# Kernel optimization log

Hardware: AMD Instinct MI355X
Metric: run time of the kernel (lower is better)

Reference implementation:

```python
import jax, jax.numpy as jnp
import numpy as np

D_MODEL, D_K, C_DIM = 1024, 64, 64
B, S = 4, 4096


def setup_inputs() -> dict:
    key = jax.random.key(0)
    ks = jax.random.split(key, 10)
    sc = 1.0 / np.sqrt(D_MODEL)
    return {
        "X": jax.random.normal(ks[0], (B, S, D_MODEL), jnp.float32),
        "cultural_embedding": jax.random.normal(ks[1], (B, C_DIM), jnp.float32),
        "WQ": jax.random.normal(ks[2], (D_MODEL, D_K), jnp.float32) * sc,
        "bQ": jnp.zeros((D_K,), jnp.float32),
        "WK": jax.random.normal(ks[3], (D_MODEL, D_K), jnp.float32) * sc,
        "bK": jnp.zeros((D_K,), jnp.float32),
        "WV": jax.random.normal(ks[4], (D_MODEL, D_K), jnp.float32) * sc,
        "bV": jnp.zeros((D_K,), jnp.float32),
        "WC": jax.random.normal(ks[5], (C_DIM, D_K), jnp.float32) * (1.0 / np.sqrt(C_DIM)),
        "bC": jnp.zeros((D_K,), jnp.float32),
        "lam": jnp.float32(1.0),
    }


def reference(X, cultural_embedding, WQ, bQ, WK, bK, WV, bV, WC, bC, lam):
    # Projections: [B,S,d_k]
    Q = jnp.einsum('bsm,mk->bsk', X, WQ) + bQ
    K = jnp.einsum('bsm,mk->bsk', X, WK) + bK
    V = jnp.einsum('bsm,mk->bsk', X, WV) + bV
    # Cultural projection: [B,d_k]
    c_proj = cultural_embedding @ WC + bC
    # Base attention logits [B,S,S]
    base_logits = jnp.einsum('bqk,bsk->bqs', Q, K) / jnp.sqrt(jnp.float32(D_K))
    # Rank-1 cultural bias per query row, scalar lambda gate
    cultural_bias = lam * jnp.einsum('bsd,bd->bs', Q, c_proj)  # [B,S]
    combined = base_logits + cultural_bias[..., None]
    attn = jax.nn.softmax(combined, axis=-1)
    return jnp.einsum('bqs,bsk->bqk', attn, V)
```

## Files before the change

kernel.cpp:

```cpp
#include <hip/hip_runtime.h>

#define B_  4
#define S_  4096
#define DM  1024
#define DK  64
#define NSPLIT 8
#define KSPAN (S_ / NSPLIT)
#define QT  256

typedef _Float16 half8  __attribute__((ext_vector_type(8)));
typedef _Float16 half4v __attribute__((ext_vector_type(4)));
typedef float    floatx4 __attribute__((ext_vector_type(4)));

#define QSCALE 0.18033688011112042f
#define EXP2F(x) __builtin_amdgcn_exp2f(x)

__global__ __launch_bounds__(256) void wt_kernel(
    const float* __restrict__ WQ, const float* __restrict__ WK,
    const float* __restrict__ WV, _Float16* __restrict__ Wt2)
{
    const int proj = blockIdx.y;
    const float* W = (proj == 0) ? WQ : (proj == 1) ? WK : WV;
    const int k0 = blockIdx.x * 64;
    const int t = threadIdx.x;
    __shared__ float T[64][68];

    #pragma unroll
    for (int p = 0; p < 4; p++) {
        int c = p * 256 + t;
        int k = c >> 4, n4 = (c & 15) * 4;
        float4 v = *(const float4*)(W + (size_t)(k0 + k) * DK + n4);
        T[k][n4 + 0] = v.x; T[k][n4 + 1] = v.y;
        T[k][n4 + 2] = v.z; T[k][n4 + 3] = v.w;
    }
    __syncthreads();

    const int n = t >> 2, kc = (t & 3) * 16;
    half8 h0, h1;
    #pragma unroll
    for (int j = 0; j < 8; j++) h0[j] = (_Float16)T[kc + j][n];
    #pragma unroll
    for (int j = 0; j < 8; j++) h1[j] = (_Float16)T[kc + 8 + j][n];
    _Float16* dst = Wt2 + (((size_t)blockIdx.x * 3 + proj) * 64 + n) * 64 + kc;
    *(half8*)(dst)     = h0;
    *(half8*)(dst + 8) = h1;
}

__global__ __launch_bounds__(256) void proj_mfma_kernel(
    const float* __restrict__ X, const _Float16* __restrict__ Wt2,
    const float* __restrict__ bQ, const float* __restrict__ bK,
    const float* __restrict__ bV,
    _Float16* __restrict__ Qh, _Float16* __restrict__ Kh,
    _Float16* __restrict__ Vt)
{
    const int t    = threadIdx.x;
    const int wave = t >> 6, lane = t & 63;
    const int quad = lane >> 4, l15 = lane & 15;
    const int row0 = blockIdx.x * 64 + wave * 16;

    const float* xp = X + (size_t)(row0 + l15) * DM + quad * 8;

    floatx4 acc[3][4];
    #pragma unroll
    for (int pr = 0; pr < 3; pr++)
        #pragma unroll
        for (int nt = 0; nt < 4; nt++)
            acc[pr][nt] = (floatx4){0.f, 0.f, 0.f, 0.f};

    float4 xa = *(const float4*)(xp + 0);
    float4 xb = *(const float4*)(xp + 4);
    float4 xc = *(const float4*)(xp + 32);
    float4 xd = *(const float4*)(xp + 36);

    for (int kt = 0; kt < DM / 64; kt++) {
        half8 xf0, xf1;
        xf0[0] = (_Float16)xa.x; xf0[1] = (_Float16)xa.y;
        xf0[2] = (_Float16)xa.z; xf0[3] = (_Float16)xa.w;
        xf0[4] = (_Float16)xb.x; xf0[5] = (_Float16)xb.y;
        xf0[6] = (_Float16)xb.z; xf0[7] = (_Float16)xb.w;
        xf1[0] = (_Float16)xc.x; xf1[1] = (_Float16)xc.y;
        xf1[2] = (_Float16)xc.z; xf1[3] = (_Float16)xc.w;
        xf1[4] = (_Float16)xd.x; xf1[5] = (_Float16)xd.y;
        xf1[6] = (_Float16)xd.z; xf1[7] = (_Float16)xd.w;

        if (kt + 1 < DM / 64) {
            const int kn = (kt + 1) * 64;
            xa = *(const float4*)(xp + kn + 0);
            xb = *(const float4*)(xp + kn + 4);
            xc = *(const float4*)(xp + kn + 32);
            xd = *(const float4*)(xp + kn + 36);
        }

        const _Float16* wb =
            Wt2 + ((size_t)kt * 3 * 64) * 64 + (size_t)l15 * 64 + quad * 8;
        #pragma unroll
        for (int pr = 0; pr < 3; pr++) {
            #pragma unroll
            for (int nt = 0; nt < 4; nt++) {
                const _Float16* wp = wb + (size_t)(pr * 64 + nt * 16) * 64;
                half8 w0 = *(const half8*)(wp);
                half8 w1 = *(const half8*)(wp + 32);
                floatx4 a = acc[pr][nt];
                a = __builtin_amdgcn_mfma_f32_16x16x32_f16(xf0, w0, a, 0, 0, 0);
                a = __builtin_amdgcn_mfma_f32_16x16x32_f16(xf1, w1, a, 0, 0, 0);
                acc[pr][nt] = a;
            }
        }
    }

    float bqv[4], bkv[4], bvv[4];
    #pragma unroll
    for (int nt = 0; nt < 4; nt++) {
        bqv[nt] = bQ[nt * 16 + l15];
        bkv[nt] = bK[nt * 16 + l15];
        bvv[nt] = bV[nt * 16 + l15];
    }

    const int orow = row0 + quad * 4;
    const int bidx = row0 >> 12;
    const int s0   = (row0 & (S_ - 1)) + quad * 4;
    #pragma unroll
    for (int nt = 0; nt < 4; nt++) {
        const int d = nt * 16 + l15;
        #pragma unroll
        for (int i = 0; i < 4; i++) {
            Qh[(size_t)(orow + i) * DK + d] =
                (_Float16)((acc[0][nt][i] + bqv[nt]) * QSCALE);
            Kh[(size_t)(orow + i) * DK + d] =
                (_Float16)(acc[1][nt][i] + bkv[nt]);
        }
        half4v hv;
        #pragma unroll
        for (int i = 0; i < 4; i++)
            hv[i] = (_Float16)(acc[2][nt][i] + bvv[nt]);
        *(half4v*)(Vt + (size_t)bidx * DK * S_ + (size_t)d * S_ + s0) = hv;
    }
}

__global__ __launch_bounds__(512, 4) void flash_mfma_kernel(
    const _Float16* __restrict__ Qh, const _Float16* __restrict__ Kh,
    const _Float16* __restrict__ Vt, _Float16* __restrict__ Oph,
    float* __restrict__ Lp)
{
    const int b     = blockIdx.y;
    const int q0    = blockIdx.x * QT;
    const int split = blockIdx.z;
    const int kbase = split * KSPAN;
    const int t     = threadIdx.x;
    const int wave  = t >> 6, lane = t & 63;
    const int quad  = lane >> 4, l15 = lane & 15;

    __shared__ __align__(16) _Float16 Ks[64 * 72];
    __shared__ __align__(16) _Float16 Vs[64 * 72];
    __shared__ __align__(16) _Float16 QsPs[QT * 72];

    const _Float16* Qb = Qh + ((size_t)b * S_ + q0) * DK;
    const _Float16* Kb = Kh + ((size_t)b * S_ + kbase) * DK;
    const _Float16* Vb = Vt + (size_t)b * DK * S_ + kbase;

    #pragma unroll
    for (int p = 0; p < 4; p++) {
        int c = p * 512 + t;
        int r = c >> 3, col = (c & 7) * 8;
        *(half8*)&QsPs[r * 72 + col] = *(const half8*)(Qb + r * 64 + col);
    }
    __syncthreads();
    half8 qf0[2], qf1[2];
    #pragma unroll
    for (int mt = 0; mt < 2; mt++) {
        const int r = wave * 32 + mt * 16 + l15;
        qf0[mt] = *(half8*)&QsPs[r * 72 + quad * 8];
        qf1[mt] = *(half8*)&QsPs[r * 72 + 32 + quad * 8];
    }
    __syncthreads();

    _Float16* Pw = &QsPs[wave * 32 * 72];

    floatx4 acc[2][4];
    float rs[2][4];
    #pragma unroll
    for (int mt = 0; mt < 2; mt++) {
        #pragma unroll
        for (int nt = 0; nt < 4; nt++) acc[mt][nt] = (floatx4){0.f,0.f,0.f,0.f};
        #pragma unroll
        for (int i = 0; i < 4; i++) rs[mt][i] = 0.f;
    }

    const int kr = t >> 3, kcol = (t & 7) * 8;
    half8 kreg = *(const half8*)(Kb + (size_t)kr * DK + kcol);
    half8 vreg = *(const half8*)(Vb + (size_t)kr * S_ + kcol);

    for (int k0 = 0; k0 < KSPAN; k0 += 64) {
        __syncthreads();
        *(half8*)&Ks[kr * 72 + kcol] = kreg;
        *(half8*)&Vs[kr * 72 + kcol] = vreg;
        __syncthreads();

        const int kn = k0 + 64;
        if (kn < KSPAN) {
            kreg = *(const half8*)(Kb + (size_t)(kn + kr) * DK + kcol);
            vreg = *(const half8*)(Vb + (size_t)kr * S_ + kn + kcol);
        }

        floatx4 sc[2][4];
        #pragma unroll
        for (int nt = 0; nt < 4; nt++) {
            half8 kf0 = *(half8*)&Ks[(nt * 16 + l15) * 72 + quad * 8];
            half8 kf1 = *(half8*)&Ks[(nt * 16 + l15) * 72 + 32 + quad * 8];
            #pragma unroll
            for (int mt = 0; mt < 2; mt++) {
                floatx4 z = (floatx4){0.f, 0.f, 0.f, 0.f};
                z = __builtin_amdgcn_mfma_f32_16x16x32_f16(qf0[mt], kf0, z, 0, 0, 0);
                z = __builtin_amdgcn_mfma_f32_16x16x32_f16(qf1[mt], kf1, z, 0, 0, 0);
                sc[mt][nt] = z;
            }
        }

        #pragma unroll
        for (int mt = 0; mt < 2; mt++)
            #pragma unroll
            for (int nt = 0; nt < 4; nt++)
                #pragma unroll
                for (int i = 0; i < 4; i++) {
                    float pe = EXP2F(sc[mt][nt][i]);
                    rs[mt][i] += pe;
                    Pw[(mt * 16 + quad * 4 + i) * 72 + nt * 16 + l15] = (_Float16)pe;
                }

        half8 pf0[2], pf1[2];
        #pragma unroll
        for (int mt = 0; mt < 2; mt++) {
            pf0[mt] = *(half8*)&Pw[(mt * 16 + l15) * 72 + quad * 8];
            pf1[mt] = *(half8*)&Pw[(mt * 16 + l15) * 72 + 32 + quad * 8];
        }

        #pragma unroll
        for (int nt = 0; nt < 4; nt++) {
            half8 vf0 = *(half8*)&Vs[(nt * 16 + l15) * 72 + quad * 8];
            half8 vf1 = *(half8*)&Vs[(nt * 16 + l15) * 72 + 32 + quad * 8];
            #pragma unroll
            for (int mt = 0; mt < 2; mt++) {
                floatx4 a = acc[mt][nt];
                a = __builtin_amdgcn_mfma_f32_16x16x32_f16(pf0[mt], vf0, a, 0, 0, 0);
                a = __builtin_amdgcn_mfma_f32_16x16x32_f16(pf1[mt], vf1, a, 0, 0, 0);
                acc[mt][nt] = a;
            }
        }
    }

    const size_t prow = (size_t)split * B_ * S_ + (size_t)b * S_ + q0;
    #pragma unroll
    for (int mt = 0; mt < 2; mt++) {
        float inv[4];
        #pragma unroll
        for (int i = 0; i < 4; i++) {
            float r = rs[mt][i];
            #pragma unroll
            for (int off = 1; off < 16; off <<= 1)
                r += __shfl_xor(r, off, 64);
            rs[mt][i] = r;
            inv[i] = 1.0f / r;
        }
        const int rbase = wave * 32 + mt * 16 + quad * 4;
        #pragma unroll
        for (int nt = 0; nt < 4; nt++)
            #pragma unroll
            for (int i = 0; i < 4; i++)
                Oph[(prow + rbase + i) * DK + nt * 16 + l15] =
                    (_Float16)(acc[mt][nt][i] * inv[i]);
        if (l15 == 0) {
            #pragma unroll
            for (int i = 0; i < 4; i++)
                Lp[prow + rbase + i] = rs[mt][i];
        }
    }
}

__global__ __launch_bounds__(256) void combine_kernel(
    const _Float16* __restrict__ Oph, const float* __restrict__ Lp,
    float* __restrict__ O)
{
    const int r  = blockIdx.x * 16 + (threadIdx.x >> 4);
    const int d4 = (threadIdx.x & 15) * 4;
    const int NR = B_ * S_;

    float lw[NSPLIT], lsum = 0.f;
    #pragma unroll
    for (int s = 0; s < NSPLIT; s++) {
        lw[s] = Lp[(size_t)s * NR + r];
        lsum += lw[s];
    }
    const float inv = 1.0f / lsum;

    float o[4] = {0.f, 0.f, 0.f, 0.f};
    #pragma unroll
    for (int s = 0; s < NSPLIT; s++) {
        half4v h = *(const half4v*)(Oph + ((size_t)s * NR + r) * DK + d4);
        const float w = lw[s];
        #pragma unroll
        for (int j = 0; j < 4; j++) o[j] += w * (float)h[j];
    }
    float4 out;
    out.x = o[0] * inv; out.y = o[1] * inv;
    out.z = o[2] * inv; out.w = o[3] * inv;
    *(float4*)(O + (size_t)r * DK + d4) = out;
}

extern "C" void kernel_launch(void* const* d_in, const int* in_sizes, int n_in,
                              void* d_out, int out_size, void* d_ws, size_t ws_size,
                              hipStream_t stream)
{
    const float* X  = (const float*)d_in[0];
    const float* WQ = (const float*)d_in[2];
    const float* bQ = (const float*)d_in[3];
    const float* WK = (const float*)d_in[4];
    const float* bK = (const float*)d_in[5];
    const float* WV = (const float*)d_in[6];
    const float* bV = (const float*)d_in[7];

    char* ws = (char*)d_ws;
    _Float16* Qh  = (_Float16*)ws;  ws += (size_t)B_ * S_ * DK * 2;
    _Float16* Kh  = (_Float16*)ws;  ws += (size_t)B_ * S_ * DK * 2;
    _Float16* Vt  = (_Float16*)ws;  ws += (size_t)B_ * S_ * DK * 2;
    _Float16* Wt2 = (_Float16*)ws;  ws += (size_t)3 * 64 * DM * 2;
    _Float16* Oph = (_Float16*)ws;  ws += (size_t)NSPLIT * B_ * S_ * DK * 2;
    float* Lp     = (float*)ws;

    wt_kernel<<<dim3(DM / 64, 3), 256, 0, stream>>>(WQ, WK, WV, Wt2);

    proj_mfma_kernel<<<dim3((B_ * S_) / 64), 256, 0, stream>>>(
        X, Wt2, bQ, bK, bV, Qh, Kh, Vt);

    flash_mfma_kernel<<<dim3(S_ / QT, B_, NSPLIT), 512, 0, stream>>>(
        Qh, Kh, Vt, Oph, Lp);

    combine_kernel<<<dim3((B_ * S_) / 16), 256, 0, stream>>>(
        Oph, Lp, (float*)d_out);
}
```

Before: 185.0 us.

## Split projection GEMM along K with fp32 partials and separate reduce kernel

The QKV projection is split into four K segments, each computed by its own block. Each block writes fp32 partial results, and a new reduce kernel sums them, adds the biases, scales Q and converts to half. This raises the number of blocks and waves available to hide X load latency. In exchange it adds large fp32 partial-buffer traffic, scattered V writes and an extra launch, and it drops the register prefetch of X.

```diff
diff --git a/kernel.cpp b/kernel.cpp
--- a/kernel.cpp
+++ b/kernel.cpp
@@ -7,6 +7,8 @@
 #define NSPLIT 8
 #define KSPAN (S_ / NSPLIT)
 #define QT  256
+#define NKS 4
+#define KSEG (DM / NKS)
 
 typedef _Float16 half8  __attribute__((ext_vector_type(8)));
 typedef _Float16 half4v __attribute__((ext_vector_type(4)));
@@ -46,19 +48,20 @@
     *(half8*)(dst + 8) = h1;
 }
 
-__global__ __launch_bounds__(256) void proj_mfma_kernel(
+__global__ __launch_bounds__(256, 4) void proj_partial_kernel(
     const float* __restrict__ X, const _Float16* __restrict__ Wt2,
-    const float* __restrict__ bQ, const float* __restrict__ bK,
-    const float* __restrict__ bV,
-    _Float16* __restrict__ Qh, _Float16* __restrict__ Kh,
-    _Float16* __restrict__ Vt)
+    float* __restrict__ Qpp, float* __restrict__ Kpp, float* __restrict__ Vpp)
 {
     const int t    = threadIdx.x;
     const int wave = t >> 6, lane = t & 63;
     const int quad = lane >> 4, l15 = lane & 15;
     const int row0 = blockIdx.x * 64 + wave * 16;
-
-    const float* xp = X + (size_t)(row0 + l15) * DM + quad * 8;
+    const int ks   = blockIdx.y;
+    const int kbase = ks * KSEG;
+
+    const float* xp = X + (size_t)(row0 + l15) * DM + kbase + quad * 8;
+    const _Float16* wb =
+        Wt2 + (size_t)(kbase / 64) * (3 * 64 * 64) + (size_t)l15 * 64 + quad * 8;
 
     floatx4 acc[3][4];
     #pragma unroll
@@ -67,12 +70,13 @@
         for (int nt = 0; nt < 4; nt++)
             acc[pr][nt] = (floatx4){0.f, 0.f, 0.f, 0.f};
 
-    float4 xa = *(const float4*)(xp + 0);
-    float4 xb = *(const float4*)(xp + 4);
-    float4 xc = *(const float4*)(xp + 32);
-    float4 xd = *(const float4*)(xp + 36);
-
-    for (int kt = 0; kt < DM / 64; kt++) {
+    for (int kt = 0; kt < KSEG / 64; kt++) {
+        const float* xpk = xp + kt * 64;
+        float4 xa = *(const float4*)(xpk + 0);
+        float4 xb = *(const float4*)(xpk + 4);
+        float4 xc = *(const float4*)(xpk + 32);
+        float4 xd = *(const float4*)(xpk + 36);
+
         half8 xf0, xf1;
         xf0[0] = (_Float16)xa.x; xf0[1] = (_Float16)xa.y;
         xf0[2] = (_Float16)xa.z; xf0[3] = (_Float16)xa.w;
@@ -83,21 +87,12 @@
         xf1[4] = (_Float16)xd.x; xf1[5] = (_Float16)xd.y;
         xf1[6] = (_Float16)xd.z; xf1[7] = (_Float16)xd.w;
 
-        if (kt + 1 < DM / 64) {
-            const int kn = (kt + 1) * 64;
-            xa = *(const float4*)(xp + kn + 0);
-            xb = *(const float4*)(xp + kn + 4);
-            xc = *(const float4*)(xp + kn + 32);
-            xd = *(const float4*)(xp + kn + 36);
-        }
-
-        const _Float16* wb =
-            Wt2 + ((size_t)kt * 3 * 64) * 64 + (size_t)l15 * 64 + quad * 8;
-        #pragma unroll
-        for (int pr = 0; pr < 3; pr++) {
+        const _Float16* wtk = wb + (size_t)kt * (3 * 64 * 64);
+        #pragma unroll
+        for (int pr = 0; pr < 3; pr++)
             #pragma unroll
             for (int nt = 0; nt < 4; nt++) {
-                const _Float16* wp = wb + (size_t)(pr * 64 + nt * 16) * 64;
+                const _Float16* wp = wtk + (pr * 64 + nt * 16) * 64;
                 half8 w0 = *(const half8*)(wp);
                 half8 w1 = *(const half8*)(wp + 32);
                 floatx4 a = acc[pr][nt];
@@ -105,35 +100,71 @@
                 a = __builtin_amdgcn_mfma_f32_16x16x32_f16(xf1, w1, a, 0, 0, 0);
                 acc[pr][nt] = a;
             }
-        }
-    }
-
-    float bqv[4], bkv[4], bvv[4];
-    #pragma unroll
-    for (int nt = 0; nt < 4; nt++) {
-        bqv[nt] = bQ[nt * 16 + l15];
-        bkv[nt] = bK[nt * 16 + l15];
-        bvv[nt] = bV[nt * 16 + l15];
-    }
-
-    const int orow = row0 + quad * 4;
-    const int bidx = row0 >> 12;
-    const int s0   = (row0 & (S_ - 1)) + quad * 4;
+    }
+
+    const size_t RC   = (size_t)B_ * S_ * DK;
+    const int    orow = row0 + quad * 4;
+    const int    bidx = row0 >> 12;
+    const int    s0   = (row0 & (S_ - 1)) + quad * 4;
+    float* Qp = Qpp + (size_t)ks * RC;
+    float* Kp = Kpp + (size_t)ks * RC;
+    float* Vp = Vpp + (size_t)ks * RC + (size_t)bidx * DK * S_;
     #pragma unroll
     for (int nt = 0; nt < 4; nt++) {
         const int d = nt * 16 + l15;
         #pragma unroll
         for (int i = 0; i < 4; i++) {
-            Qh[(size_t)(orow + i) * DK + d] =
-                (_Float16)((acc[0][nt][i] + bqv[nt]) * QSCALE);
-            Kh[(size_t)(orow + i) * DK + d] =
-                (_Float16)(acc[1][nt][i] + bkv[nt]);
-        }
-        half4v hv;
-        #pragma unroll
-        for (int i = 0; i < 4; i++)
-            hv[i] = (_Float16)(acc[2][nt][i] + bvv[nt]);
-        *(half4v*)(Vt + (size_t)bidx * DK * S_ + (size_t)d * S_ + s0) = hv;
+            Qp[(size_t)(orow + i) * DK + d] = acc[0][nt][i];
+            Kp[(size_t)(orow + i) * DK + d] = acc[1][nt][i];
+            Vp[(size_t)d * S_ + s0 + i]     = acc[2][nt][i];
+        }
+    }
+}
+
+__global__ __launch_bounds__(256) void proj_reduce_kernel(
+    const float* __restrict__ Qpp, const float* __restrict__ Kpp,
+    const float* __restrict__ Vpp,
+    const float* __restrict__ bQ, const float* __restrict__ bK,
+    const float* __restrict__ bV,
+    _Float16* __restrict__ Qh, _Float16* __restrict__ Kh,
+    _Float16* __restrict__ Vt)
+{
+    const int which = blockIdx.y;
+    const size_t RC = (size_t)B_ * S_ * DK;
+    const size_t idx = ((size_t)blockIdx.x * 256 + threadIdx.x) * 4;
+
+    const float* Pp = (which == 0) ? Qpp : (which == 1) ? Kpp : Vpp;
+
+    float4 s = *(const float4*)(Pp + idx);
+    #pragma unroll
+    for (int ks = 1; ks < NKS; ks++) {
+        float4 p = *(const float4*)(Pp + (size_t)ks * RC + idx);
+        s.x += p.x; s.y += p.y; s.z += p.z; s.w += p.w;
+    }
+
+    half4v h;
+    if (which == 0) {
+        const int d4 = (int)(idx & 63);
+        h[0] = (_Float16)((s.x + bQ[d4 + 0]) * QSCALE);
+        h[1] = (_Float16)((s.y + bQ[d4 + 1]) * QSCALE);
+        h[2] = (_Float16)((s.z + bQ[d4 + 2]) * QSCALE);
+        h[3] = (_Float16)((s.w + bQ[d4 + 3]) * QSCALE);
+        *(half4v*)(Qh + idx) = h;
+    } else if (which == 1) {
+        const int d4 = (int)(idx & 63);
+        h[0] = (_Float16)(s.x + bK[d4 + 0]);
+        h[1] = (_Float16)(s.y + bK[d4 + 1]);
+        h[2] = (_Float16)(s.z + bK[d4 + 2]);
+        h[3] = (_Float16)(s.w + bK[d4 + 3]);
+        *(half4v*)(Kh + idx) = h;
+    } else {
+        const int d = (int)((idx >> 12) & 63);
+        const float bv = bV[d];
+        h[0] = (_Float16)(s.x + bv);
+        h[1] = (_Float16)(s.y + bv);
+        h[2] = (_Float16)(s.z + bv);
+        h[3] = (_Float16)(s.w + bv);
+        *(half4v*)(Vt + idx) = h;
     }
 }
 
@@ -324,12 +355,18 @@
     _Float16* Vt  = (_Float16*)ws;  ws += (size_t)B_ * S_ * DK * 2;
     _Float16* Wt2 = (_Float16*)ws;  ws += (size_t)3 * 64 * DM * 2;
     _Float16* Oph = (_Float16*)ws;  ws += (size_t)NSPLIT * B_ * S_ * DK * 2;
-    float* Lp     = (float*)ws;
+    float* Lp     = (float*)ws;     ws += (size_t)NSPLIT * B_ * S_ * 4;
+    float* Qpp    = (float*)ws;     ws += (size_t)NKS * B_ * S_ * DK * 4;
+    float* Kpp    = (float*)ws;     ws += (size_t)NKS * B_ * S_ * DK * 4;
+    float* Vpp    = (float*)ws;     ws += (size_t)NKS * B_ * S_ * DK * 4;
 
     wt_kernel<<<dim3(DM / 64, 3), 256, 0, stream>>>(WQ, WK, WV, Wt2);
 
-    proj_mfma_kernel<<<dim3((B_ * S_) / 64), 256, 0, stream>>>(
-        X, Wt2, bQ, bK, bV, Qh, Kh, Vt);
+    proj_partial_kernel<<<dim3((B_ * S_) / 64, NKS), 256, 0, stream>>>(
+        X, Wt2, Qpp, Kpp, Vpp);
+
+    proj_reduce_kernel<<<dim3((B_ * S_ * DK) / 1024, 3), 256, 0, stream>>>(
+        Qpp, Kpp, Vpp, bQ, bK, bV, Qh, Kh, Vt);
 
     flash_mfma_kernel<<<dim3(S_ / QT, B_, NSPLIT), 512, 0, stream>>>(
         Qh, Kh, Vt, Oph, Lp);
```

After: 204.0 us. 10.2% more time.

## Stage projection tiles in LDS and split Q/K/V across waves

Applied to the files above, without the earlier changes.

The projection kernel now stages each 64-wide K-slice of X (converted to fp16) and all three weight tiles in shared memory, double-buffered through registers. Each block covers 32 rows with 6 waves, one per (projection, row-group) pair, so each wave keeps only 4 accumulators instead of 12. Before, every wave read its weight fragments straight from global memory. The change is meant to cut redundant global weight traffic and register pressure, which should allow more resident waves. The cost is two barriers per K-step and LDS traffic.

```diff
diff --git a/kernel.cpp b/kernel.cpp
--- a/kernel.cpp
+++ b/kernel.cpp
@@ -46,7 +46,7 @@
     *(half8*)(dst + 8) = h1;
 }
 
-__global__ __launch_bounds__(256) void proj_mfma_kernel(
+__global__ __launch_bounds__(384, 3) void proj_kernel(
     const float* __restrict__ X, const _Float16* __restrict__ Wt2,
     const float* __restrict__ bQ, const float* __restrict__ bK,
     const float* __restrict__ bV,
@@ -56,84 +56,111 @@
     const int t    = threadIdx.x;
     const int wave = t >> 6, lane = t & 63;
     const int quad = lane >> 4, l15 = lane & 15;
-    const int row0 = blockIdx.x * 64 + wave * 16;
-
-    const float* xp = X + (size_t)(row0 + l15) * DM + quad * 8;
-
-    floatx4 acc[3][4];
-    #pragma unroll
-    for (int pr = 0; pr < 3; pr++)
+    const int pr   = wave % 3;
+    const int rg   = wave / 3;
+    const int row0 = blockIdx.x * 32;
+
+    __shared__ __align__(16) _Float16 Xs[32 * 72];
+    __shared__ __align__(16) _Float16 Ws[3][64 * 72];
+
+    floatx4 acc[4];
+    #pragma unroll
+    for (int nt = 0; nt < 4; nt++) acc[nt] = (floatx4){0.f, 0.f, 0.f, 0.f};
+
+    const int xr_ = t >> 3, xc_ = (t & 7) * 8;
+    int wpr_[4], wn_[4], wc_[4];
+    #pragma unroll
+    for (int p = 0; p < 4; p++) {
+        int c = p * 384 + t;
+        int n_lin = c >> 3;
+        wpr_[p] = n_lin >> 6; wn_[p] = n_lin & 63; wc_[p] = (c & 7) * 8;
+    }
+
+    float4 xreg0, xreg1;
+    half8  wreg[4];
+    if (t < 256) {
+        const float* src = X + (size_t)(row0 + xr_) * DM + xc_;
+        xreg0 = *(const float4*)(src);
+        xreg1 = *(const float4*)(src + 4);
+    }
+    #pragma unroll
+    for (int p = 0; p < 4; p++)
+        wreg[p] = *(const half8*)(Wt2 +
+            ((size_t)wpr_[p] * 64 + wn_[p]) * 64 + wc_[p]);
+
+    for (int kt = 0; kt < DM / 64; kt++) {
+        __syncthreads();
+        if (t < 256) {
+            half8 h;
+            #pragma unroll
+            for (int j = 0; j < 4; j++) h[j]     = (_Float16)xreg0[j];
+            #pragma unroll
+            for (int j = 0; j < 4; j++) h[4 + j] = (_Float16)xreg1[j];
+            *(half8*)&Xs[xr_ * 72 + xc_] = h;
+        }
+        #pragma unroll
+        for (int p = 0; p < 4; p++)
+            *(half8*)&Ws[wpr_[p]][wn_[p] * 72 + wc_[p]] = wreg[p];
+        __syncthreads();
+
+        if (kt + 1 < DM / 64) {
+            const int kg = (kt + 1) * 64;
+            if (t < 256) {
+                const float* src = X + (size_t)(row0 + xr_) * DM + kg + xc_;
+                xreg0 = *(const float4*)(src);
+                xreg1 = *(const float4*)(src + 4);
+            }
+            #pragma unroll
+            for (int p = 0; p < 4; p++)
+                wreg[p] = *(const half8*)(Wt2 +
+                    (((size_t)(kt + 1) * 3 + wpr_[p]) * 64 + wn_[p]) * 64 + wc_[p]);
+        }
+
+        half8 xf0 = *(half8*)&Xs[(rg * 16 + l15) * 72 + quad * 8];
+        half8 xf1 = *(half8*)&Xs[(rg * 16 + l15) * 72 + 32 + quad * 8];
+        #pragma unroll
+        for (int nt = 0; nt < 4; nt++) {
+            half8 wf0 = *(half8*)&Ws[pr][(nt * 16 + l15) * 72 + quad * 8];
+            half8 wf1 = *(half8*)&Ws[pr][(nt * 16 + l15) * 72 + 32 + quad * 8];
+            floatx4 a = acc[nt];
+            a = __builtin_amdgcn_mfma_f32_16x16x32_f16(xf0, wf0, a, 0, 0, 0);
+            a = __builtin_amdgcn_mfma_f32_16x16x32_f16(xf1, wf1, a, 0, 0, 0);
+            acc[nt] = a;
+        }
+    }
+
+    const float* bias = (pr == 0) ? bQ : (pr == 1) ? bK : bV;
+    float bv[4];
+    #pragma unroll
+    for (int nt = 0; nt < 4; nt++) bv[nt] = bias[nt * 16 + l15];
+
+    const int orow = row0 + rg * 16 + quad * 4;
+    if (pr == 0) {
         #pragma unroll
         for (int nt = 0; nt < 4; nt++)
-            acc[pr][nt] = (floatx4){0.f, 0.f, 0.f, 0.f};
-
-    float4 xa = *(const float4*)(xp + 0);
-    float4 xb = *(const float4*)(xp + 4);
-    float4 xc = *(const float4*)(xp + 32);
-    float4 xd = *(const float4*)(xp + 36);
-
-    for (int kt = 0; kt < DM / 64; kt++) {
-        half8 xf0, xf1;
-        xf0[0] = (_Float16)xa.x; xf0[1] = (_Float16)xa.y;
-        xf0[2] = (_Float16)xa.z; xf0[3] = (_Float16)xa.w;
-        xf0[4] = (_Float16)xb.x; xf0[5] = (_Float16)xb.y;
-        xf0[6] = (_Float16)xb.z; xf0[7] = (_Float16)xb.w;
-        xf1[0] = (_Float16)xc.x; xf1[1] = (_Float16)xc.y;
-        xf1[2] = (_Float16)xc.z; xf1[3] = (_Float16)xc.w;
-        xf1[4] = (_Float16)xd.x; xf1[5] = (_Float16)xd.y;
-        xf1[6] = (_Float16)xd.z; xf1[7] = (_Float16)xd.w;
-
-        if (kt + 1 < DM / 64) {
-            const int kn = (kt + 1) * 64;
-            xa = *(const float4*)(xp + kn + 0);
-            xb = *(const float4*)(xp + kn + 4);
-            xc = *(const float4*)(xp + kn + 32);
-            xd = *(const float4*)(xp + kn + 36);
-        }
-
-        const _Float16* wb =
-            Wt2 + ((size_t)kt * 3 * 64) * 64 + (size_t)l15 * 64 + quad * 8;
-        #pragma unroll
-        for (int pr = 0; pr < 3; pr++) {
-            #pragma unroll
-            for (int nt = 0; nt < 4; nt++) {
-                const _Float16* wp = wb + (size_t)(pr * 64 + nt * 16) * 64;
-                half8 w0 = *(const half8*)(wp);
-                half8 w1 = *(const half8*)(wp + 32);
-                floatx4 a = acc[pr][nt];
-                a = __builtin_amdgcn_mfma_f32_16x16x32_f16(xf0, w0, a, 0, 0, 0);
-                a = __builtin_amdgcn_mfma_f32_16x16x32_f16(xf1, w1, a, 0, 0, 0);
-                acc[pr][nt] = a;
-            }
-        }
-    }
-
-    float bqv[4], bkv[4], bvv[4];
-    #pragma unroll
-    for (int nt = 0; nt < 4; nt++) {
-        bqv[nt] = bQ[nt * 16 + l15];
-        bkv[nt] = bK[nt * 16 + l15];
-        bvv[nt] = bV[nt * 16 + l15];
-    }
-
-    const int orow = row0 + quad * 4;
-    const int bidx = row0 >> 12;
-    const int s0   = (row0 & (S_ - 1)) + quad * 4;
-    #pragma unroll
-    for (int nt = 0; nt < 4; nt++) {
-        const int d = nt * 16 + l15;
-        #pragma unroll
-        for (int i = 0; i < 4; i++) {
-            Qh[(size_t)(orow + i) * DK + d] =
-                (_Float16)((acc[0][nt][i] + bqv[nt]) * QSCALE);
-            Kh[(size_t)(orow + i) * DK + d] =
-                (_Float16)(acc[1][nt][i] + bkv[nt]);
-        }
-        half4v hv;
-        #pragma unroll
-        for (int i = 0; i < 4; i++)
-            hv[i] = (_Float16)(acc[2][nt][i] + bvv[nt]);
-        *(half4v*)(Vt + (size_t)bidx * DK * S_ + (size_t)d * S_ + s0) = hv;
+            #pragma unroll
+            for (int i = 0; i < 4; i++)
+                Qh[(size_t)(orow + i) * DK + nt * 16 + l15] =
+                    (_Float16)((acc[nt][i] + bv[nt]) * QSCALE);
+    } else if (pr == 1) {
+        #pragma unroll
+        for (int nt = 0; nt < 4; nt++)
+            #pragma unroll
+            for (int i = 0; i < 4; i++)
+                Kh[(size_t)(orow + i) * DK + nt * 16 + l15] =
+                    (_Float16)(acc[nt][i] + bv[nt]);
+    } else {
+        const int bidx = row0 >> 12;
+        const int s0   = (row0 & (S_ - 1)) + rg * 16 + quad * 4;
+        #pragma unroll
+        for (int nt = 0; nt < 4; nt++) {
+            half4v hv;
+            #pragma unroll
+            for (int i = 0; i < 4; i++)
+                hv[i] = (_Float16)(acc[nt][i] + bv[nt]);
+            *(half4v*)(Vt + (size_t)bidx * DK * S_ +
+                       (size_t)(nt * 16 + l15) * S_ + s0) = hv;
+        }
     }
 }
 
@@ -328,7 +355,7 @@
 
     wt_kernel<<<dim3(DM / 64, 3), 256, 0, stream>>>(WQ, WK, WV, Wt2);
 
-    proj_mfma_kernel<<<dim3((B_ * S_) / 64), 256, 0, stream>>>(
+    proj_kernel<<<dim3((B_ * S_) / 32), 384, 0, stream>>>(
         X, Wt2, bQ, bK, bV, Qh, Kh, Vt);
 
     flash_mfma_kernel<<<dim3(S_ / QT, B_, NSPLIT), 512, 0, stream>>>(
```

Result: faster. 158.0 us (-14.6%).
